# Performance work log

Hardware: AMD Instinct MI355X
Metric: run time of the kernel (lower is better)

The kernel has to match this reference:

```python
import jax, jax.numpy as jnp
import numpy as np
from jax import lax

DIM = 384
NH = 8
HD = DIM // NH
M = 16          # num_anchors
B = 16
HH = 64
WW = 64
N = HH * WW
STD = 0.02


def setup_inputs() -> dict:
    key = jax.random.key(0)
    ks = jax.random.split(key, 12)
    rn = lambda k, shape: (jax.random.normal(k, shape, jnp.float32) * STD)
    return {
        "x": jax.random.normal(ks[0], (B, N, DIM), jnp.float32),
        "H": HH,
        "W": WW,
        "saliency_w": rn(ks[1], (DIM, 1)),
        "saliency_b": jnp.zeros((1,), jnp.float32),
        "anchor_seeds": rn(ks[2], (1, M, DIM)),
        "w_q_agg": rn(ks[3], (DIM, DIM)),
        "w_kv_agg": rn(ks[4], (DIM, 2 * DIM)),
        "w_q_self": rn(ks[5], (DIM, DIM)),
        "w_kv_self": rn(ks[6], (DIM, 2 * DIM)),
        "w_q_bcast": rn(ks[7], (DIM, DIM)),
        "w_kv_bcast": rn(ks[8], (DIM, 2 * DIM)),
        "dw_kernel": rn(ks[9], (DIM, 1, 3, 3)),  # depthwise conv, OIHW with I=1
        "w_proj": rn(ks[10], (DIM, DIM)),
    }


def _mhsa(q_in, kv_in, wq, wkv):
    """Multi-head cross attention. q_in: [B,Lq,C], kv_in: [B,Lk,C]."""
    b, lq, c = q_in.shape
    lk = kv_in.shape[1]
    scale = HD ** -0.5
    q = (q_in @ wq).reshape(b, lq, NH, HD)
    kv = (kv_in @ wkv).reshape(b, lk, 2, NH, HD)
    k, v = kv[:, :, 0], kv[:, :, 1]
    attn = jnp.einsum("bqhd,bkhd->bhqk", q, k) * scale
    attn = jax.nn.softmax(attn, axis=-1)
    out = jnp.einsum("bhqk,bkhd->bqhd", attn, v).reshape(b, lq, c)
    return out


def reference(x, H, W, saliency_w, saliency_b, anchor_seeds,
              w_q_agg, w_kv_agg, w_q_self, w_kv_self,
              w_q_bcast, w_kv_bcast, dw_kernel, w_proj):
    b, n, c = x.shape
    # saliency gating
    sal = jax.nn.sigmoid(x @ saliency_w + saliency_b)  # [B,N,1]
    x_sal = x * sal
    # stage 1: anchors aggregate from saliency-gated tokens
    anchors = jnp.broadcast_to(anchor_seeds, (b, M, c))
    anchors = anchors + _mhsa(anchors, x_sal, w_q_agg, w_kv_agg)
    # stage 2: anchor self-attention
    anchors = anchors + _mhsa(anchors, anchors, w_q_self, w_kv_self)
    # stage 3: broadcast anchors back to all tokens
    global_out = _mhsa(x, anchors, w_q_bcast, w_kv_bcast)
    # depthwise 3x3 conv on the 2D token map
    x2d = x.reshape(b, H, W, c).transpose(0, 3, 1, 2)  # NCHW
    local = lax.conv_general_dilated(
        x2d, dw_kernel, window_strides=(1, 1), padding="SAME",
        feature_group_count=c,
        dimension_numbers=("NCHW", "OIHW", "NCHW"))
    local = local.transpose(0, 2, 3, 1).reshape(b, n, c)
    return (global_out + local) @ w_proj
```

## Files before the change

kernel.cpp:

```cpp
#include <hip/hip_runtime.h>
#include <hip/hip_bf16.h>

#define SCALE 0.14433756729740643f

typedef __attribute__((ext_vector_type(8))) short bf16x8;
typedef __attribute__((ext_vector_type(4))) float f32x4;

template <typename T> __device__ inline T cvt_from_f(float v);
template <> __device__ inline float cvt_from_f<float>(float v) { return v; }
template <> __device__ inline __hip_bfloat16 cvt_from_f<__hip_bfloat16>(float v) { return __float2bfloat16(v); }

__device__ inline void gload16(const void* g, void* l) {
  __builtin_amdgcn_global_load_lds((const __attribute__((address_space(1))) void*)g,
                                   (__attribute__((address_space(3))) void*)l, 16, 0, 0);
}

__device__ inline int xcd_flat(int nwg) {
  int flat = (blockIdx.z * gridDim.y + blockIdx.y) * gridDim.x + blockIdx.x;
  int per = nwg >> 3;
  return (flat & 7) * per + (flat >> 3);
}

__global__ __launch_bounds__(256) void prep(const float* __restrict__ x,
                                            const float* __restrict__ wsal,
                                            const float* __restrict__ bsal,
                                            __hip_bfloat16* __restrict__ xb,
                                            float* __restrict__ sal) {
  int wave = threadIdx.x >> 6, lane = threadIdx.x & 63;
  size_t row = (size_t)blockIdx.x * 4 + wave;
  const float* xr = x + row * 384;
  float xs[6];
  float part = 0.f;
#pragma unroll
  for (int j = 0; j < 6; j++) {
    int c = lane + 64 * j;
    xs[j] = xr[c];
    part += xs[j] * wsal[c];
  }
#pragma unroll
  for (int off = 32; off >= 1; off >>= 1) part += __shfl_xor(part, off);
  float s = 1.f / (1.f + __expf(-(part + bsal[0])));
#pragma unroll
  for (int j = 0; j < 6; j++) {
    int c = lane + 64 * j;
    xb[row * 384 + c] = __float2bfloat16(xs[j]);
  }
  if (lane == 0) sal[row] = s;
}

__global__ __launch_bounds__(256) void xtrans(const __hip_bfloat16* __restrict__ xb,
                                              __hip_bfloat16* __restrict__ xbT) {
  __shared__ short t[64][66];
  int n0 = blockIdx.x * 64, c0 = blockIdx.y * 64, b = blockIdx.z;
  int tid = threadIdx.x;
  int r = tid >> 3, c8 = tid & 7;
#pragma unroll
  for (int i = 0; i < 2; i++) {
    int row = r + i * 32;
    bf16x8 v = *(const bf16x8*)(xb + ((size_t)(b * 4096 + n0 + row)) * 384 + c0 + c8 * 8);
    unsigned int* trow = (unsigned int*)&t[row][c8 * 8];
#pragma unroll
    for (int j = 0; j < 4; j++) {
      union { unsigned int u; short s[2]; } p;
      p.s[0] = v[j * 2];
      p.s[1] = v[j * 2 + 1];
      trow[j] = p.u;
    }
  }
  __syncthreads();
#pragma unroll
  for (int i = 0; i < 2; i++) {
    int crow = r + i * 32;
    short tb[8];
#pragma unroll
    for (int j = 0; j < 8; j++) tb[j] = t[c8 * 8 + j][crow];
    *(ulonglong2*)(xbT + ((size_t)b * 384 + c0 + crow) * 4096 + n0 + c8 * 8) = *(ulonglong2*)tb;
  }
}

__global__ __launch_bounds__(256) void weights_prep(const float* __restrict__ wkv,
                                                    const float* __restrict__ wproj,
                                                    const float* __restrict__ seeds,
                                                    const float* __restrict__ wqagg,
                                                    __hip_bfloat16* __restrict__ wvlT,
                                                    __hip_bfloat16* __restrict__ bt2,
                                                    float* __restrict__ qseed) {
  __shared__ float shbuf[16 * 385];
  int bx = blockIdx.x;
  int tid = threadIdx.x;
  if (bx < 576) {
    int idx = bx * 256 + tid;
    if (idx < 384 * 384) {
      int n = idx / 384, k = idx % 384;
      wvlT[idx] = __float2bfloat16(wkv[(size_t)k * 768 + 384 + n]);
    }
  } else if (bx < 720) {
    int bx2 = bx - 576;
    int xt = bx2 % 6, yt = (bx2 / 6) % 6, zb = bx2 / 36;
    float(*t)[65] = (float(*)[65])shbuf;
    int kt = xt * 64, ct = yt * 64;
    int c = tid & 63, r4 = tid >> 6;
#pragma unroll
    for (int i = 0; i < 16; i++) {
      int r = i * 4 + r4;
      t[r][c] = wproj[(size_t)(kt + r) * 384 + ct + c];
    }
    __syncthreads();
    __hip_bfloat16 vals[16];
#pragma unroll
    for (int i = 0; i < 16; i++) vals[i] = __float2bfloat16(t[c][i * 4 + r4]);
    for (int b = zb * 4; b < zb * 4 + 4; b++) {
      __hip_bfloat16* dst = bt2 + (size_t)b * 196608;
#pragma unroll
      for (int i = 0; i < 16; i++) {
        int rr = i * 4 + r4;
        dst[(size_t)(ct + rr) * 512 + kt + c] = vals[i];
      }
    }
  } else {
    int bxq = bx - 720;
    float(*a1)[385] = (float(*)[385])shbuf;
    int cs = bxq * 16;
    for (int idx = tid; idx < 6144; idx += 256) a1[idx / 384][idx % 384] = seeds[idx];
    __syncthreads();
    int m = tid >> 4, cc = tid & 15;
    int col = cs + cc;
    const float* wp = wqagg + col;
    float acc0 = 0.f, acc1 = 0.f, acc2 = 0.f, acc3 = 0.f;
#pragma unroll 4
    for (int k = 0; k < 384; k += 4) {
      acc0 += a1[m][k] * wp[(size_t)k * 384];
      acc1 += a1[m][k + 1] * wp[(size_t)(k + 1) * 384];
      acc2 += a1[m][k + 2] * wp[(size_t)(k + 2) * 384];
      acc3 += a1[m][k + 3] * wp[(size_t)(k + 3) * 384];
    }
    qseed[m * 384 + col] = ((acc0 + acc1) + (acc2 + acc3)) * SCALE;
  }
}

template <int K, typename OT, int BSHIFT>
__global__ __launch_bounds__(256) void gemm_mfma(const __hip_bfloat16* __restrict__ A,
                                                 const __hip_bfloat16* __restrict__ BT,
                                                 OT* __restrict__ out, int Ncols,
                                                 size_t btBatchStride) {
  __shared__ __align__(16) __hip_bfloat16 Asl[128][32];
  __shared__ __align__(16) __hip_bfloat16 Bsl[128][32];
  int nf = xcd_flat(gridDim.x * gridDim.y);
  int bX = nf % gridDim.x, bY = nf / gridDim.x;
  int tid = threadIdx.x;
  int lane = tid & 63;
  int w = tid >> 6;
  int wr = w >> 1, wc = w & 1;
  int fr = lane & 15, fq = lane >> 4;
  int rowBase = bY * 128, colBase = bX * 128;
  const __hip_bfloat16* BTb = BT + (size_t)(rowBase >> BSHIFT) * btBatchStride;

  int r1 = tid >> 2, kc1 = tid & 3;
  int r2 = (tid + 256) >> 2;

  char* aB1 = (char*)Asl + (size_t)(w * 64) * 16;
  char* aB2 = (char*)Asl + (size_t)(256 + w * 64) * 16;
  char* bB1 = (char*)Bsl + (size_t)(w * 64) * 16;
  char* bB2 = (char*)Bsl + (size_t)(256 + w * 64) * 16;

  const __hip_bfloat16* a1 = A + (size_t)(rowBase + r1) * K + kc1 * 8;
  const __hip_bfloat16* a2 = A + (size_t)(rowBase + r2) * K + kc1 * 8;
  const __hip_bfloat16* b1 = BTb + (size_t)(colBase + r1) * K + kc1 * 8;
  const __hip_bfloat16* b2 = BTb + (size_t)(colBase + r2) * K + kc1 * 8;

  f32x4 acc[4][4] = {};

  for (int kk = 0; kk < K; kk += 32) {
    gload16(a1 + kk, aB1);
    gload16(a2 + kk, aB2);
    gload16(b1 + kk, bB1);
    gload16(b2 + kk, bB2);
    __syncthreads();
    bf16x8 af[4], bfv[4];
#pragma unroll
    for (int m = 0; m < 4; m++) af[m] = *(const bf16x8*)&Asl[wr * 64 + m * 16 + fr][fq * 8];
#pragma unroll
    for (int n = 0; n < 4; n++) bfv[n] = *(const bf16x8*)&Bsl[wc * 64 + n * 16 + fr][fq * 8];
#pragma unroll
    for (int m = 0; m < 4; m++)
#pragma unroll
      for (int n = 0; n < 4; n++)
        acc[m][n] = __builtin_amdgcn_mfma_f32_16x16x32_bf16(af[m], bfv[n], acc[m][n], 0, 0, 0);
    __syncthreads();
  }

#pragma unroll
  for (int m = 0; m < 4; m++) {
    int row0 = rowBase + wr * 64 + m * 16 + fq * 4;
#pragma unroll
    for (int n = 0; n < 4; n++) {
      int col = colBase + wc * 64 + n * 16 + fr;
      f32x4 v = acc[m][n];
#pragma unroll
      for (int r = 0; r < 4; r++) out[(size_t)(row0 + r) * Ncols + col] = cvt_from_f<OT>(v[r]);
    }
  }
}

__global__ __launch_bounds__(256) void gemm_out(const __hip_bfloat16* __restrict__ A,
                                                const __hip_bfloat16* __restrict__ BT,
                                                float* __restrict__ out) {
  __shared__ __align__(16) __hip_bfloat16 Asl[128][64];
  __shared__ __align__(16) __hip_bfloat16 Bsl[128][64];
  int nf = xcd_flat(1536);
  int bX = nf % 3, bY = nf / 3;
  int tid = threadIdx.x;
  int lane = tid & 63;
  int w = tid >> 6;
  int wr = w >> 1, wc = w & 1;
  int fr = lane & 15, fq = lane >> 4;
  int rowBase = bY * 128, colBase = bX * 128;
  const __hip_bfloat16* BTb = BT + (size_t)(rowBase >> 12) * (384 * 512);

  int r0 = tid >> 3, jc = tid & 7;
  int kc = jc ^ (r0 & 7);
  char* aB[4];
  char* bB[4];
  const __hip_bfloat16* a_src[4];
  const __hip_bfloat16* b_src[4];
#pragma unroll
  for (int i = 0; i < 4; i++) {
    aB[i] = (char*)Asl + (size_t)(i * 256 + w * 64) * 16;
    bB[i] = (char*)Bsl + (size_t)(i * 256 + w * 64) * 16;
    a_src[i] = A + (size_t)(rowBase + r0 + i * 32) * 512 + kc * 8;
    b_src[i] = BTb + (size_t)(colBase + r0 + i * 32) * 512 + kc * 8;
  }

  f32x4 acc[4][4] = {};

  for (int kk = 0; kk < 512; kk += 64) {
#pragma unroll
    for (int i = 0; i < 4; i++) {
      gload16(a_src[i] + kk, aB[i]);
      gload16(b_src[i] + kk, bB[i]);
    }
    __syncthreads();
#pragma unroll
    for (int half = 0; half < 2; half++) {
      bf16x8 af[4], bfv[4];
#pragma unroll
      for (int m = 0; m < 4; m++) {
        int row = wr * 64 + m * 16 + fr;
        af[m] = *(const bf16x8*)((char*)Asl + (size_t)row * 128 +
                                 (((fq + 4 * half) ^ (row & 7)) << 4));
      }
#pragma unroll
      for (int n = 0; n < 4; n++) {
        int row = wc * 64 + n * 16 + fr;
        bfv[n] = *(const bf16x8*)((char*)Bsl + (size_t)row * 128 +
                                  (((fq + 4 * half) ^ (row & 7)) << 4));
      }
#pragma unroll
      for (int m = 0; m < 4; m++)
#pragma unroll
        for (int n = 0; n < 4; n++)
          acc[m][n] = __builtin_amdgcn_mfma_f32_16x16x32_bf16(af[m], bfv[n], acc[m][n], 0, 0, 0);
    }
    __syncthreads();
  }

#pragma unroll
  for (int m = 0; m < 4; m++) {
    int row0 = rowBase + wr * 64 + m * 16 + fq * 4;
#pragma unroll
    for (int n = 0; n < 4; n++) {
      int col = colBase + wc * 64 + n * 16 + fr;
      f32x4 v = acc[m][n];
#pragma unroll
      for (int r = 0; r < 4; r++) out[(size_t)(row0 + r) * 384 + col] = v[r];
    }
  }
}

__global__ __launch_bounds__(256) void gemm_logits(const __hip_bfloat16* __restrict__ A,
                                                   const __hip_bfloat16* __restrict__ BT,
                                                   __hip_bfloat16* __restrict__ lgT,
                                                   const float* __restrict__ rowScale) {
  __shared__ __align__(16) __hip_bfloat16 Asl[128][64];
  __shared__ __align__(16) __hip_bfloat16 Bsl[128][64];
  int tid = threadIdx.x;
  int lane = tid & 63;
  int w = tid >> 6;
  int wr = w >> 1, wc = w & 1;
  int fr = lane & 15, fq = lane >> 4;
  int rowBase = blockIdx.x * 128;

  int r0 = tid >> 3, jc = tid & 7;
  int kc = jc ^ (r0 & 7);
  char* aB[4];
  char* bB[4];
  const __hip_bfloat16* a_src[4];
  const __hip_bfloat16* b_src[4];
#pragma unroll
  for (int i = 0; i < 4; i++) {
    aB[i] = (char*)Asl + (size_t)(i * 256 + w * 64) * 16;
    bB[i] = (char*)Bsl + (size_t)(i * 256 + w * 64) * 16;
    a_src[i] = A + (size_t)(rowBase + r0 + i * 32) * 384 + kc * 8;
    b_src[i] = BT + (size_t)(r0 + i * 32) * 384 + kc * 8;
  }

  f32x4 acc[4][4] = {};

  for (int kk = 0; kk < 384; kk += 64) {
#pragma unroll
    for (int i = 0; i < 4; i++) {
      gload16(a_src[i] + kk, aB[i]);
      gload16(b_src[i] + kk, bB[i]);
    }
    __syncthreads();
#pragma unroll
    for (int half = 0; half < 2; half++) {
      bf16x8 af[4], bfv[4];
#pragma unroll
      for (int m = 0; m < 4; m++) {
        int row = wr * 64 + m * 16 + fr;
        af[m] = *(const bf16x8*)((char*)Asl + (size_t)row * 128 +
                                 (((fq + 4 * half) ^ (row & 7)) << 4));
      }
#pragma unroll
      for (int n = 0; n < 4; n++) {
        int row = wc * 64 + n * 16 + fr;
        bfv[n] = *(const bf16x8*)((char*)Bsl + (size_t)row * 128 +
                                  (((fq + 4 * half) ^ (row & 7)) << 4));
      }
#pragma unroll
      for (int m = 0; m < 4; m++)
#pragma unroll
        for (int n = 0; n < 4; n++)
          acc[m][n] = __builtin_amdgcn_mfma_f32_16x16x32_bf16(af[m], bfv[n], acc[m][n], 0, 0, 0);
    }
    __syncthreads();
  }

  float sv[4][4];
#pragma unroll
  for (int m = 0; m < 4; m++)
#pragma unroll
    for (int r = 0; r < 4; r++)
      sv[m][r] = rowScale[rowBase + wr * 64 + m * 16 + fq * 4 + r];

#pragma unroll
  for (int m = 0; m < 4; m++) {
    int row0 = rowBase + wr * 64 + m * 16 + fq * 4;
    int bb = row0 >> 12;
    int n0 = row0 & 4095;
#pragma unroll
    for (int n = 0; n < 4; n++) {
      int col = wc * 64 + n * 16 + fr;
      __hip_bfloat16 tb[4];
#pragma unroll
      for (int r = 0; r < 4; r++) tb[r] = __float2bfloat16(acc[m][n][r] * sv[m][r]);
      *(unsigned long long*)(lgT + ((size_t)bb * 128 + col) * 4096 + n0) = *(unsigned long long*)tb;
    }
  }
}

__global__ __launch_bounds__(256) void softmax_rows(const __hip_bfloat16* __restrict__ lgT,
                                                    const float* __restrict__ sal,
                                                    __hip_bfloat16* __restrict__ PT) {
  int g = blockIdx.x;
  const __hip_bfloat16* row = lgT + (size_t)g * 4096;
  int tid = threadIdx.x, wv = tid >> 6, lane = tid & 63;
  __shared__ float redm[4], reds[4];
  float v[16];
  union { ulonglong2 u; __hip_bfloat16 h[8]; } L0, L1;
  L0.u = *(const ulonglong2*)(row + tid * 16);
  L1.u = *(const ulonglong2*)(row + tid * 16 + 8);
#pragma unroll
  for (int i = 0; i < 8; i++) {
    v[i] = __bfloat162float(L0.h[i]);
    v[8 + i] = __bfloat162float(L1.h[i]);
  }
  float mx = v[0];
#pragma unroll
  for (int i = 1; i < 16; i++) mx = fmaxf(mx, v[i]);
#pragma unroll
  for (int off = 1; off < 64; off <<= 1) mx = fmaxf(mx, __shfl_xor(mx, off));
  if (lane == 0) redm[wv] = mx;
  __syncthreads();
  mx = fmaxf(fmaxf(redm[0], redm[1]), fmaxf(redm[2], redm[3]));
  float s = 0.f;
#pragma unroll
  for (int i = 0; i < 16; i++) {
    v[i] = __expf(v[i] - mx);
    s += v[i];
  }
#pragma unroll
  for (int off = 1; off < 64; off <<= 1) s += __shfl_xor(s, off);
  if (lane == 0) reds[wv] = s;
  __syncthreads();
  s = (reds[0] + reds[1]) + (reds[2] + reds[3]);
  float inv = 1.f / s;
  const float* sp = sal + (size_t)(g >> 7) * 4096 + tid * 16;
  float salv[16];
#pragma unroll
  for (int i = 0; i < 4; i++) {
    float4 q = *(const float4*)(sp + i * 4);
    salv[i * 4] = q.x; salv[i * 4 + 1] = q.y; salv[i * 4 + 2] = q.z; salv[i * 4 + 3] = q.w;
  }
  __hip_bfloat16 tb[16];
#pragma unroll
  for (int i = 0; i < 16; i++) tb[i] = __float2bfloat16(v[i] * inv * salv[i]);
  __hip_bfloat16* op = PT + (size_t)g * 4096 + tid * 16;
  *(ulonglong2*)op = *(ulonglong2*)tb;
  *(ulonglong2*)(op + 8) = *(ulonglong2*)(tb + 8);
}

__global__ __launch_bounds__(256) void gemm_pvx(const __hip_bfloat16* __restrict__ PT,
                                                const __hip_bfloat16* __restrict__ xbT,
                                                float* __restrict__ pbuf) {
  __shared__ __align__(16) __hip_bfloat16 Asl[128][64];
  __shared__ __align__(16) __hip_bfloat16 Bsl[128][64];
  int nf = xcd_flat(192);
  int bX = nf % 3, bY = (nf / 3) & 15, kz = nf / 48;
  int tid = threadIdx.x;
  int lane = tid & 63;
  int w = tid >> 6;
  int wr = w >> 1, wc = w & 1;
  int fr = lane & 15, fq = lane >> 4;
  int rowBase = bY * 128, colBase = bX * 128;
  const __hip_bfloat16* BTb = xbT + (size_t)bY * 384 * 4096;

  int r0 = tid >> 3, jc = tid & 7;
  int kc = jc ^ (r0 & 7);
  char* aB[4];
  char* bB[4];
  const __hip_bfloat16* a_src[4];
  const __hip_bfloat16* b_src[4];
#pragma unroll
  for (int i = 0; i < 4; i++) {
    aB[i] = (char*)Asl + (size_t)(i * 256 + w * 64) * 16;
    bB[i] = (char*)Bsl + (size_t)(i * 256 + w * 64) * 16;
    a_src[i] = PT + (size_t)(rowBase + r0 + i * 32) * 4096 + kz * 1024 + kc * 8;
    b_src[i] = BTb + (size_t)(colBase + r0 + i * 32) * 4096 + kz * 1024 + kc * 8;
  }

  f32x4 acc[4][4] = {};

  for (int kk = 0; kk < 1024; kk += 64) {
#pragma unroll
    for (int i = 0; i < 4; i++) {
      gload16(a_src[i] + kk, aB[i]);
      gload16(b_src[i] + kk, bB[i]);
    }
    __syncthreads();
#pragma unroll
    for (int half = 0; half < 2; half++) {
      bf16x8 af[4], bfv[4];
#pragma unroll
      for (int m = 0; m < 4; m++) {
        int row = wr * 64 + m * 16 + fr;
        af[m] = *(const bf16x8*)((char*)Asl + (size_t)row * 128 +
                                 (((fq + 4 * half) ^ (row & 7)) << 4));
      }
#pragma unroll
      for (int n = 0; n < 4; n++) {
        int row = wc * 64 + n * 16 + fr;
        bfv[n] = *(const bf16x8*)((char*)Bsl + (size_t)row * 128 +
                                  (((fq + 4 * half) ^ (row & 7)) << 4));
      }
#pragma unroll
      for (int m = 0; m < 4; m++)
#pragma unroll
        for (int n = 0; n < 4; n++)
          acc[m][n] = __builtin_amdgcn_mfma_f32_16x16x32_bf16(af[m], bfv[n], acc[m][n], 0, 0, 0);
    }
    __syncthreads();
  }

  float* outz = pbuf + (size_t)kz * 786432;
#pragma unroll
  for (int m = 0; m < 4; m++) {
    int row0 = rowBase + wr * 64 + m * 16 + fq * 4;
#pragma unroll
    for (int n = 0; n < 4; n++) {
      int col = colBase + wc * 64 + n * 16 + fr;
      f32x4 v = acc[m][n];
#pragma unroll
      for (int r = 0; r < 4; r++) outz[(size_t)(row0 + r) * 384 + col] = v[r];
    }
  }
}

__global__ __launch_bounds__(256) void reduce_z(const float* __restrict__ pbuf,
                                                __hip_bfloat16* __restrict__ pvx) {
  int i4 = (blockIdx.x * 256 + threadIdx.x) * 4;
  float4 s = *(const float4*)(pbuf + i4);
#pragma unroll
  for (int z = 1; z < 4; z++) {
    float4 t = *(const float4*)(pbuf + (size_t)z * 786432 + i4);
    s.x += t.x; s.y += t.y; s.z += t.z; s.w += t.w;
  }
  __hip_bfloat16 tb[4] = {__float2bfloat16(s.x), __float2bfloat16(s.y),
                          __float2bfloat16(s.z), __float2bfloat16(s.w)};
  *(unsigned long long*)(pvx + i4) = *(unsigned long long*)tb;
}

__global__ void anch_fix(const float* __restrict__ outF, const float* __restrict__ seeds,
                         float* __restrict__ anch1) {
  int idx = blockIdx.x * 256 + threadIdx.x;
  int b = idx / 6144;
  int rem = idx - b * 6144;
  int m = rem / 384, c = rem - m * 384;
  int h = c / 48;
  anch1[idx] = seeds[rem] + outF[((size_t)b * 128 + h * 16 + m) * 384 + c];
}

__global__ void fill_wl(const float* __restrict__ wkv, const float* __restrict__ qseed,
                        __hip_bfloat16* __restrict__ wvlT) {
  int idx = blockIdx.x * 256 + threadIdx.x;
  int hm = idx / 384, ci = idx - hm * 384;
  int h = hm >> 4, m = hm & 15;
  const float* wp = wkv + (size_t)ci * 768 + h * 48;
  const float* qp = qseed + m * 384 + h * 48;
  float acc = 0.f;
#pragma unroll
  for (int d = 0; d < 48; d++) acc += wp[d] * qp[d];
  wvlT[384 * 384 + idx] = __float2bfloat16(acc);
}

__global__ __launch_bounds__(256) void kvfold(const float* __restrict__ anch2,
                                              const float* __restrict__ wkvb,
                                              const float* __restrict__ wq,
                                              const float* __restrict__ wproj,
                                              __hip_bfloat16* __restrict__ wpbT,
                                              __hip_bfloat16* __restrict__ bt2) {
  int b = blockIdx.y;
  int tid = threadIdx.x;
  __shared__ float a2s[16][385];
  __shared__ float stage[16][48];
  __shared__ __hip_bfloat16 obuf[16][264];
  bool isK = blockIdx.x < 8;
  int h = isK ? blockIdx.x : blockIdx.x - 8;
  int colBase = (isK ? 0 : 384) + h * 48;
  float scale = isK ? SCALE : 1.f;
  for (int idx = tid; idx < 6144; idx += 256) a2s[idx / 384][idx % 384] = anch2[b * 6144 + idx];
  __syncthreads();
  for (int o = tid; o < 768; o += 256) {
    int m = o / 48, d = o - m * 48;
    const float* wp = wkvb + colBase + d;
    float acc0 = 0.f, acc1 = 0.f, acc2 = 0.f, acc3 = 0.f;
#pragma unroll 4
    for (int k = 0; k < 384; k += 4) {
      acc0 += a2s[m][k] * wp[(size_t)k * 768];
      acc1 += a2s[m][k + 1] * wp[(size_t)(k + 1) * 768];
      acc2 += a2s[m][k + 2] * wp[(size_t)(k + 2) * 768];
      acc3 += a2s[m][k + 3] * wp[(size_t)(k + 3) * 768];
    }
    stage[m][d] = ((acc0 + acc1) + (acc2 + acc3)) * scale;
  }
  __syncthreads();
  if (isK) {
    for (int kbase = 0; kbase < 384; kbase += 256) {
      int chunk = (kbase == 0) ? 256 : 128;
      if (tid < chunk) {
        int k = kbase + tid;
        const float4* wp = (const float4*)(wq + (size_t)k * 384 + h * 48);
        float acc[16] = {};
#pragma unroll
        for (int dq = 0; dq < 12; dq++) {
          float4 wv = wp[dq];
#pragma unroll
          for (int m = 0; m < 16; m++)
            acc[m] += stage[m][dq * 4] * wv.x + stage[m][dq * 4 + 1] * wv.y +
                      stage[m][dq * 4 + 2] * wv.z + stage[m][dq * 4 + 3] * wv.w;
        }
#pragma unroll
        for (int m = 0; m < 16; m++) obuf[m][tid] = __float2bfloat16(acc[m]);
      }
      __syncthreads();
      for (int widx = tid; widx < 16 * chunk; widx += 256) {
        int m = widx / chunk, kk = widx - m * chunk;
        wpbT[(size_t)b * 49152 + (size_t)(h * 16 + m) * 384 + kbase + kk] = obuf[m][kk];
      }
      __syncthreads();
    }
  } else {
    for (int cp = tid; cp < 384; cp += 256) {
      float acc[16] = {};
      for (int d = 0; d < 48; d++) {
        float wv = wproj[(size_t)(h * 48 + d) * 384 + cp];
#pragma unroll
        for (int m = 0; m < 16; m++) acc[m] += stage[m][d] * wv;
      }
      __hip_bfloat16 tb[16];
#pragma unroll
      for (int m = 0; m < 16; m++) tb[m] = __float2bfloat16(acc[m]);
      __hip_bfloat16* dst = bt2 + (size_t)b * 196608 + (size_t)cp * 512 + 384 + h * 16;
      *(ulonglong2*)dst = *(ulonglong2*)tb;
      *(ulonglong2*)(dst + 8) = *(ulonglong2*)(tb + 8);
    }
  }
}

__global__ __launch_bounds__(256) void pgemm(const __hip_bfloat16* __restrict__ A,
                                             const __hip_bfloat16* __restrict__ wpbT,
                                             __hip_bfloat16* __restrict__ A2) {
  __shared__ __align__(16) __hip_bfloat16 Asl[128][64];
  __shared__ __align__(16) __hip_bfloat16 Bsl[128][64];
  int tid = threadIdx.x;
  int lane = tid & 63;
  int w = tid >> 6;
  int wr = w >> 1, wc = w & 1;
  int fr = lane & 15, fq = lane >> 4;
  int rowBase = blockIdx.x * 128;
  const __hip_bfloat16* BTb = wpbT + (size_t)(rowBase >> 12) * (128 * 384);

  int r0 = tid >> 3, jc = tid & 7;
  int kc = jc ^ (r0 & 7);
  char* aB[4];
  char* bB[4];
  const __hip_bfloat16* a_src[4];
  const __hip_bfloat16* b_src[4];
#pragma unroll
  for (int i = 0; i < 4; i++) {
    aB[i] = (char*)Asl + (size_t)(i * 256 + w * 64) * 16;
    bB[i] = (char*)Bsl + (size_t)(i * 256 + w * 64) * 16;
    a_src[i] = A + (size_t)(rowBase + r0 + i * 32) * 384 + kc * 8;
    b_src[i] = BTb + (size_t)(r0 + i * 32) * 384 + kc * 8;
  }

  f32x4 acc[4][4] = {};

  for (int kk = 0; kk < 384; kk += 64) {
#pragma unroll
    for (int i = 0; i < 4; i++) {
      gload16(a_src[i] + kk, aB[i]);
      gload16(b_src[i] + kk, bB[i]);
    }
    __syncthreads();
#pragma unroll
    for (int half = 0; half < 2; half++) {
      bf16x8 af[4], bfv[4];
#pragma unroll
      for (int m = 0; m < 4; m++) {
        int row = wr * 64 + m * 16 + fr;
        af[m] = *(const bf16x8*)((char*)Asl + (size_t)row * 128 +
                                 (((fq + 4 * half) ^ (row & 7)) << 4));
      }
#pragma unroll
      for (int n = 0; n < 4; n++) {
        int row = wc * 64 + n * 16 + fr;
        bfv[n] = *(const bf16x8*)((char*)Bsl + (size_t)row * 128 +
                                  (((fq + 4 * half) ^ (row & 7)) << 4));
      }
#pragma unroll
      for (int m = 0; m < 4; m++)
#pragma unroll
        for (int n = 0; n < 4; n++)
          acc[m][n] = __builtin_amdgcn_mfma_f32_16x16x32_bf16(af[m], bfv[n], acc[m][n], 0, 0, 0);
    }
    __syncthreads();
  }

#pragma unroll
  for (int m = 0; m < 4; m++) {
    int row0 = rowBase + wr * 64 + m * 16 + fq * 4;
#pragma unroll
    for (int n = 0; n < 4; n++) {
      int col = wc * 64 + n * 16 + fr;
      f32x4 v = acc[m][n];
      f32x4 mx = v;
#pragma unroll
      for (int off = 1; off < 16; off <<= 1)
#pragma unroll
        for (int r = 0; r < 4; r++) mx[r] = fmaxf(mx[r], __shfl_xor(mx[r], off));
      f32x4 e;
#pragma unroll
      for (int r = 0; r < 4; r++) e[r] = __expf(v[r] - mx[r]);
      f32x4 s = e;
#pragma unroll
      for (int off = 1; off < 16; off <<= 1)
#pragma unroll
        for (int r = 0; r < 4; r++) s[r] += __shfl_xor(s[r], off);
#pragma unroll
      for (int r = 0; r < 4; r++)
        A2[(size_t)(row0 + r) * 512 + 384 + col] = __float2bfloat16(e[r] / s[r]);
    }
  }
}

__global__ __launch_bounds__(256) void dwconv3(const __hip_bfloat16* __restrict__ xb,
                                               const float* __restrict__ dwk,
                                               __hip_bfloat16* __restrict__ A2) {
  int b = blockIdx.y;
  int y = blockIdx.x;
  int w = threadIdx.x >> 6, lane = threadIdx.x & 63;
  int c0 = lane * 6;
  int x0 = w * 16;
  float kw[9][6];
#pragma unroll
  for (int ki = 0; ki < 9; ki++)
#pragma unroll
    for (int i = 0; i < 6; i++) kw[ki][i] = dwk[(c0 + i) * 9 + ki];

  const __hip_bfloat16* base = xb + ((size_t)(b * 4096 + y * 64)) * 384 + c0;
  bool yv[3];
#pragma unroll
  for (int t = 0; t < 3; t++) {
    int yy = y + t - 1;
    yv[t] = (yy >= 0 && yy < 64);
  }

  float colL[3][6], colC[3][6], colR[3][6];
  auto loadcol = [&](float (&dst)[3][6], int x) {
#pragma unroll
    for (int t = 0; t < 3; t++) {
      if (yv[t]) {
        const __hip_bfloat16* p = base + ((size_t)(t - 1) * 64 + x) * 384;
#pragma unroll
        for (int i = 0; i < 6; i++) dst[t][i] = __bfloat162float(p[i]);
      } else {
#pragma unroll
        for (int i = 0; i < 6; i++) dst[t][i] = 0.f;
      }
    }
  };

  if (x0 == 0) {
#pragma unroll
    for (int t = 0; t < 3; t++)
#pragma unroll
      for (int i = 0; i < 6; i++) colL[t][i] = 0.f;
  } else {
    loadcol(colL, x0 - 1);
  }
  loadcol(colC, x0);

  for (int step = 0; step < 16; step++) {
    int x = x0 + step;
    if (x + 1 < 64) {
      loadcol(colR, x + 1);
    } else {
#pragma unroll
      for (int t = 0; t < 3; t++)
#pragma unroll
        for (int i = 0; i < 6; i++) colR[t][i] = 0.f;
    }
    float acc[6];
#pragma unroll
    for (int i = 0; i < 6; i++) {
      float a = 0.f;
#pragma unroll
      for (int t = 0; t < 3; t++)
        a += colL[t][i] * kw[t * 3 + 0][i] + colC[t][i] * kw[t * 3 + 1][i] +
             colR[t][i] * kw[t * 3 + 2][i];
      acc[i] = a;
    }
    __hip_bfloat16 tb[6];
#pragma unroll
    for (int i = 0; i < 6; i++) tb[i] = __float2bfloat16(acc[i]);
    __hip_bfloat16* gp = A2 + ((size_t)(b * 4096 + y * 64 + x)) * 512 + c0;
    *(unsigned int*)(gp) = *(unsigned int*)(tb);
    *(unsigned int*)(gp + 2) = *(unsigned int*)(tb + 2);
    *(unsigned int*)(gp + 4) = *(unsigned int*)(tb + 4);
#pragma unroll
    for (int t = 0; t < 3; t++)
#pragma unroll
      for (int i = 0; i < 6; i++) {
        colL[t][i] = colC[t][i];
        colC[t][i] = colR[t][i];
      }
  }
}

__global__ __launch_bounds__(256) void anchor_proj_qkv(const float* __restrict__ A,
                                                       const float* __restrict__ Wq,
                                                       const float* __restrict__ Wkv,
                                                       float* __restrict__ q_out,
                                                       float* __restrict__ kv_out) {
  bool isQ = blockIdx.x < 24;
  int bx = isQ ? blockIdx.x : blockIdx.x - 24;
  const float* W = isQ ? Wq : Wkv;
  float* outp = isQ ? q_out : kv_out;
  int wstride = isQ ? 384 : 768;
  float scale = isQ ? SCALE : 1.f;
  int cs = bx * 16;
  int b = blockIdx.y;
  __shared__ float a1[16][385];
  int tid = threadIdx.x;
  for (int idx = tid; idx < 6144; idx += 256) a1[idx / 384][idx % 384] = A[b * 6144 + idx];
  __syncthreads();
  int m = tid >> 4, cc = tid & 15;
  int col = cs + cc;
  const float* wp = W + col;
  float acc0 = 0.f, acc1 = 0.f, acc2 = 0.f, acc3 = 0.f;
#pragma unroll 4
  for (int k = 0; k < 384; k += 4) {
    acc0 += a1[m][k] * wp[(size_t)k * wstride];
    acc1 += a1[m][k + 1] * wp[(size_t)(k + 1) * wstride];
    acc2 += a1[m][k + 2] * wp[(size_t)(k + 2) * wstride];
    acc3 += a1[m][k + 3] * wp[(size_t)(k + 3) * wstride];
  }
  float acc = ((acc0 + acc1) + (acc2 + acc3)) * scale;
  outp[((size_t)b * 16 + m) * wstride + col] = acc;
}

__global__ void self_attn(const float* __restrict__ qsf, const float* __restrict__ kvs,
                          const float* __restrict__ anch1, float* __restrict__ anch2) {
  int h = blockIdx.x & 7, b = blockIdx.x >> 3;
  __shared__ float qs[16][48], ks[16][48], vs[16][48], p[16][17];
  int tid = threadIdx.x;
  for (int idx = tid; idx < 768; idx += 256) {
    int m = idx / 48, d = idx % 48;
    qs[m][d] = qsf[(b * 16 + m) * 384 + h * 48 + d];
    ks[m][d] = kvs[(b * 16 + m) * 768 + h * 48 + d];
    vs[m][d] = kvs[(b * 16 + m) * 768 + 384 + h * 48 + d];
  }
  __syncthreads();
  {
    int mq = tid >> 4, mk = tid & 15;
    float acc = 0.f;
    for (int d = 0; d < 48; d++) acc += qs[mq][d] * ks[mk][d];
    p[mq][mk] = acc;
  }
  __syncthreads();
  if (tid < 16) {
    float mx = -1e30f;
    for (int mk = 0; mk < 16; mk++) mx = fmaxf(mx, p[tid][mk]);
    float sum = 0.f;
    for (int mk = 0; mk < 16; mk++) {
      float e = __expf(p[tid][mk] - mx);
      p[tid][mk] = e;
      sum += e;
    }
    float inv = 1.f / sum;
    for (int mk = 0; mk < 16; mk++) p[tid][mk] *= inv;
  }
  __syncthreads();
  for (int idx = tid; idx < 768; idx += 256) {
    int m = idx / 48, d = idx % 48;
    float acc = 0.f;
    for (int mk = 0; mk < 16; mk++) acc += p[m][mk] * vs[mk][d];
    int c = h * 48 + d;
    anch2[(b * 16 + m) * 384 + c] = anch1[(b * 16 + m) * 384 + c] + acc;
  }
}

extern "C" void kernel_launch(void* const* d_in, const int* in_sizes, int n_in,
                              void* d_out, int out_size, void* d_ws, size_t ws_size,
                              hipStream_t stream) {
  (void)in_sizes; (void)n_in; (void)out_size; (void)ws_size;
  const float* x = (const float*)d_in[0];
  const float* wsal = (const float*)d_in[3];
  const float* bsal = (const float*)d_in[4];
  const float* seeds = (const float*)d_in[5];
  const float* w_q_agg = (const float*)d_in[6];
  const float* w_kv_agg = (const float*)d_in[7];
  const float* w_q_self = (const float*)d_in[8];
  const float* w_kv_self = (const float*)d_in[9];
  const float* w_q_bcast = (const float*)d_in[10];
  const float* w_kv_bcast = (const float*)d_in[11];
  const float* dwk = (const float*)d_in[12];
  const float* w_proj = (const float*)d_in[13];
  float* out = (float*)d_out;

  char* ws = (char*)d_ws;
  size_t off = 0;
  auto take = [&](size_t bytes) -> void* {
    void* p = ws + off;
    off += (bytes + 255) & ~(size_t)255;
    return p;
  };
  __hip_bfloat16* xb = (__hip_bfloat16*)take(50331648);
  __hip_bfloat16* xbT = (__hip_bfloat16*)take(50331648);
  char* R = (char*)take(67108864);
  __hip_bfloat16* PT = (__hip_bfloat16*)take(16777216);
  __hip_bfloat16* pvx = (__hip_bfloat16*)take(1572864);
  float* outF = (float*)take(3145728);
  float* qseed = (float*)take(24576);
  float* sal = (float*)take(262144);
  float* anch1 = (float*)take(393216);
  float* anch2 = (float*)take(393216);
  float* q_self = (float*)take(393216);
  float* kv_self = (float*)take(786432);
  __hip_bfloat16* wvlT = (__hip_bfloat16*)take(393216);
  __hip_bfloat16* wpbT = (__hip_bfloat16*)take(1572864);
  __hip_bfloat16* bt2 = (__hip_bfloat16*)take(6291456);
  __hip_bfloat16* logitsT = (__hip_bfloat16*)R;
  float* pbuf = (float*)R;
  __hip_bfloat16* A2 = (__hip_bfloat16*)R;

  prep<<<16384, 256, 0, stream>>>(x, wsal, bsal, xb, sal);
  xtrans<<<dim3(64, 6, 16), 256, 0, stream>>>(xb, xbT);
  weights_prep<<<744, 256, 0, stream>>>(w_kv_agg, w_proj, seeds, w_q_agg, wvlT, bt2, qseed);
  fill_wl<<<192, 256, 0, stream>>>(w_kv_agg, qseed, wvlT);
  gemm_logits<<<512, 256, 0, stream>>>(xb, wvlT + 384 * 384, logitsT, sal);
  softmax_rows<<<2048, 256, 0, stream>>>(logitsT, sal, PT);
  gemm_pvx<<<dim3(3, 16, 4), 256, 0, stream>>>(PT, xbT, pbuf);
  reduce_z<<<768, 256, 0, stream>>>(pbuf, pvx);
  gemm_mfma<384, float, 12><<<dim3(3, 16), 256, 0, stream>>>(pvx, wvlT, outF, 384, 0);
  anch_fix<<<384, 256, 0, stream>>>(outF, seeds, anch1);
  anchor_proj_qkv<<<dim3(72, 16), 256, 0, stream>>>(anch1, w_q_self, w_kv_self, q_self, kv_self);
  self_attn<<<128, 256, 0, stream>>>(q_self, kv_self, anch1, anch2);
  kvfold<<<dim3(16, 16), 256, 0, stream>>>(anch2, w_kv_bcast, w_q_bcast, w_proj, wpbT, bt2);
  pgemm<<<512, 256, 0, stream>>>(xb, wpbT, A2);
  dwconv3<<<dim3(64, 16), 256, 0, stream>>>(xb, dwk, A2);
  gemm_out<<<dim3(3, 512), 256, 0, stream>>>(A2, bt2, out);
}
```

Baseline: 320.2 us.

## Merge independent kernels into shared launches to cut launch count

```diff
diff --git a/kernel.cpp b/kernel.cpp
--- a/kernel.cpp
+++ b/kernel.cpp
@@ -48,44 +48,14 @@
   if (lane == 0) sal[row] = s;
 }
 
-__global__ __launch_bounds__(256) void xtrans(const __hip_bfloat16* __restrict__ xb,
-                                              __hip_bfloat16* __restrict__ xbT) {
-  __shared__ short t[64][66];
-  int n0 = blockIdx.x * 64, c0 = blockIdx.y * 64, b = blockIdx.z;
-  int tid = threadIdx.x;
-  int r = tid >> 3, c8 = tid & 7;
-#pragma unroll
-  for (int i = 0; i < 2; i++) {
-    int row = r + i * 32;
-    bf16x8 v = *(const bf16x8*)(xb + ((size_t)(b * 4096 + n0 + row)) * 384 + c0 + c8 * 8);
-    unsigned int* trow = (unsigned int*)&t[row][c8 * 8];
-#pragma unroll
-    for (int j = 0; j < 4; j++) {
-      union { unsigned int u; short s[2]; } p;
-      p.s[0] = v[j * 2];
-      p.s[1] = v[j * 2 + 1];
-      trow[j] = p.u;
-    }
-  }
-  __syncthreads();
-#pragma unroll
-  for (int i = 0; i < 2; i++) {
-    int crow = r + i * 32;
-    short tb[8];
-#pragma unroll
-    for (int j = 0; j < 8; j++) tb[j] = t[c8 * 8 + j][crow];
-    *(ulonglong2*)(xbT + ((size_t)b * 384 + c0 + crow) * 4096 + n0 + c8 * 8) = *(ulonglong2*)tb;
-  }
-}
-
 __global__ __launch_bounds__(256) void weights_prep(const float* __restrict__ wkv,
                                                     const float* __restrict__ wproj,
                                                     const float* __restrict__ seeds,
                                                     const float* __restrict__ wqagg,
                                                     __hip_bfloat16* __restrict__ wvlT,
-                                                    __hip_bfloat16* __restrict__ bt2,
-                                                    float* __restrict__ qseed) {
+                                                    __hip_bfloat16* __restrict__ bt2) {
   __shared__ float shbuf[16 * 385];
+  __shared__ float qsl[16][48];
   int bx = blockIdx.x;
   int tid = threadIdx.x;
   if (bx < 576) {
@@ -118,23 +88,29 @@
       }
     }
   } else {
-    int bxq = bx - 720;
+    int h = bx - 720;
     float(*a1)[385] = (float(*)[385])shbuf;
-    int cs = bxq * 16;
     for (int idx = tid; idx < 6144; idx += 256) a1[idx / 384][idx % 384] = seeds[idx];
     __syncthreads();
-    int m = tid >> 4, cc = tid & 15;
-    int col = cs + cc;
-    const float* wp = wqagg + col;
-    float acc0 = 0.f, acc1 = 0.f, acc2 = 0.f, acc3 = 0.f;
-#pragma unroll 4
-    for (int k = 0; k < 384; k += 4) {
-      acc0 += a1[m][k] * wp[(size_t)k * 384];
-      acc1 += a1[m][k + 1] * wp[(size_t)(k + 1) * 384];
-      acc2 += a1[m][k + 2] * wp[(size_t)(k + 2) * 384];
-      acc3 += a1[m][k + 3] * wp[(size_t)(k + 3) * 384];
-    }
-    qseed[m * 384 + col] = ((acc0 + acc1) + (acc2 + acc3)) * SCALE;
+    for (int o = tid; o < 768; o += 256) {
+      int m = o / 48, d = o - m * 48;
+      const float* wp = wqagg + h * 48 + d;
+      float acc0 = 0.f, acc1 = 0.f;
+      for (int k = 0; k < 384; k += 2) {
+        acc0 += a1[m][k] * wp[(size_t)k * 384];
+        acc1 += a1[m][k + 1] * wp[(size_t)(k + 1) * 384];
+      }
+      qsl[m][d] = (acc0 + acc1) * SCALE;
+    }
+    __syncthreads();
+    for (int idx = tid; idx < 6144; idx += 256) {
+      int m = idx / 384, ci = idx - m * 384;
+      const float* wp = wkv + (size_t)ci * 768 + h * 48;
+      float acc = 0.f;
+#pragma unroll
+      for (int d = 0; d < 48; d++) acc += wp[d] * qsl[m][d];
+      wvlT[384 * 384 + (size_t)(h * 16 + m) * 384 + ci] = __float2bfloat16(acc);
+    }
   }
 }
 
@@ -277,13 +253,45 @@
   }
 }
 
-__global__ __launch_bounds__(256) void gemm_logits(const __hip_bfloat16* __restrict__ A,
-                                                   const __hip_bfloat16* __restrict__ BT,
-                                                   __hip_bfloat16* __restrict__ lgT,
-                                                   const float* __restrict__ rowScale) {
+__global__ __launch_bounds__(256) void glx(const __hip_bfloat16* __restrict__ A,
+                                           const __hip_bfloat16* __restrict__ BT,
+                                           __hip_bfloat16* __restrict__ lgT,
+                                           const float* __restrict__ rowScale,
+                                           __hip_bfloat16* __restrict__ xbT) {
   __shared__ __align__(16) __hip_bfloat16 Asl[128][64];
   __shared__ __align__(16) __hip_bfloat16 Bsl[128][64];
   int tid = threadIdx.x;
+  if (blockIdx.x >= 512) {
+    int b2 = blockIdx.x - 512;
+    int n0 = (b2 & 63) * 64;
+    int c0 = ((b2 >> 6) % 6) * 64;
+    int b = b2 / 384;
+    short(*t)[66] = (short(*)[66])Asl;
+    int r = tid >> 3, c8 = tid & 7;
+#pragma unroll
+    for (int i = 0; i < 2; i++) {
+      int row = r + i * 32;
+      bf16x8 v = *(const bf16x8*)(A + ((size_t)(b * 4096 + n0 + row)) * 384 + c0 + c8 * 8);
+      unsigned int* trow = (unsigned int*)&t[row][c8 * 8];
+#pragma unroll
+      for (int j = 0; j < 4; j++) {
+        union { unsigned int u; short s[2]; } p;
+        p.s[0] = v[j * 2];
+        p.s[1] = v[j * 2 + 1];
+        trow[j] = p.u;
+      }
+    }
+    __syncthreads();
+#pragma unroll
+    for (int i = 0; i < 2; i++) {
+      int crow = r + i * 32;
+      short tb[8];
+#pragma unroll
+      for (int j = 0; j < 8; j++) tb[j] = t[c8 * 8 + j][crow];
+      *(ulonglong2*)(xbT + ((size_t)b * 384 + c0 + crow) * 4096 + n0 + c8 * 8) = *(ulonglong2*)tb;
+    }
+    return;
+  }
   int lane = tid & 63;
   int w = tid >> 6;
   int wr = w >> 1, wc = w & 1;
@@ -509,19 +517,6 @@
   int m = rem / 384, c = rem - m * 384;
   int h = c / 48;
   anch1[idx] = seeds[rem] + outF[((size_t)b * 128 + h * 16 + m) * 384 + c];
-}
-
-__global__ void fill_wl(const float* __restrict__ wkv, const float* __restrict__ qseed,
-                        __hip_bfloat16* __restrict__ wvlT) {
-  int idx = blockIdx.x * 256 + threadIdx.x;
-  int hm = idx / 384, ci = idx - hm * 384;
-  int h = hm >> 4, m = hm & 15;
-  const float* wp = wkv + (size_t)ci * 768 + h * 48;
-  const float* qp = qseed + m * 384 + h * 48;
-  float acc = 0.f;
-#pragma unroll
-  for (int d = 0; d < 48; d++) acc += wp[d] * qp[d];
-  wvlT[384 * 384 + idx] = __float2bfloat16(acc);
 }
 
 __global__ __launch_bounds__(256) void kvfold(const float* __restrict__ anch2,
@@ -598,12 +593,95 @@
   }
 }
 
-__global__ __launch_bounds__(256) void pgemm(const __hip_bfloat16* __restrict__ A,
-                                             const __hip_bfloat16* __restrict__ wpbT,
-                                             __hip_bfloat16* __restrict__ A2) {
+__global__ __launch_bounds__(256) void pgemm_dw(const __hip_bfloat16* __restrict__ A,
+                                                const __hip_bfloat16* __restrict__ wpbT,
+                                                const float* __restrict__ dwk,
+                                                __hip_bfloat16* __restrict__ A2) {
   __shared__ __align__(16) __hip_bfloat16 Asl[128][64];
   __shared__ __align__(16) __hip_bfloat16 Bsl[128][64];
   int tid = threadIdx.x;
+  if (blockIdx.x >= 512) {
+    int b2 = blockIdx.x - 512;
+    int y = b2 & 63, b = b2 >> 6;
+    int w = tid >> 6, lane = tid & 63;
+    int c0 = lane * 6;
+    int x0 = w * 16;
+    float kw[9][6];
+#pragma unroll
+    for (int ki = 0; ki < 9; ki++)
+#pragma unroll
+      for (int i = 0; i < 6; i++) kw[ki][i] = dwk[(c0 + i) * 9 + ki];
+
+    const __hip_bfloat16* base = A + ((size_t)(b * 4096 + y * 64)) * 384 + c0;
+    bool yv[3];
+#pragma unroll
+    for (int t = 0; t < 3; t++) {
+      int yy = y + t - 1;
+      yv[t] = (yy >= 0 && yy < 64);
+    }
+
+    float colL[3][6], colC[3][6], colR[3][6];
+    auto loadcol = [&](float (&dst)[3][6], int x) {
+#pragma unroll
+      for (int t = 0; t < 3; t++) {
+        if (yv[t]) {
+          const __hip_bfloat16* p = base + ((size_t)(t - 1) * 64 + x) * 384;
+#pragma unroll
+          for (int i = 0; i < 6; i++) dst[t][i] = __bfloat162float(p[i]);
+        } else {
+#pragma unroll
+          for (int i = 0; i < 6; i++) dst[t][i] = 0.f;
+        }
+      }
+    };
+
+    if (x0 == 0) {
+#pragma unroll
+      for (int t = 0; t < 3; t++)
+#pragma unroll
+        for (int i = 0; i < 6; i++) colL[t][i] = 0.f;
+    } else {
+      loadcol(colL, x0 - 1);
+    }
+    loadcol(colC, x0);
+
+    for (int step = 0; step < 16; step++) {
+      int x = x0 + step;
+      if (x + 1 < 64) {
+        loadcol(colR, x + 1);
+      } else {
+#pragma unroll
+        for (int t = 0; t < 3; t++)
+#pragma unroll
+          for (int i = 0; i < 6; i++) colR[t][i] = 0.f;
+      }
+      float acc[6];
+#pragma unroll
+      for (int i = 0; i < 6; i++) {
+        float a = 0.f;
+#pragma unroll
+        for (int t = 0; t < 3; t++)
+          a += colL[t][i] * kw[t * 3 + 0][i] + colC[t][i] * kw[t * 3 + 1][i] +
+               colR[t][i] * kw[t * 3 + 2][i];
+        acc[i] = a;
+      }
+      __hip_bfloat16 tb[6];
+#pragma unroll
+      for (int i = 0; i < 6; i++) tb[i] = __float2bfloat16(acc[i]);
+      __hip_bfloat16* gp = A2 + ((size_t)(b * 4096 + y * 64 + x)) * 512 + c0;
+      *(unsigned int*)(gp) = *(unsigned int*)(tb);
+      *(unsigned int*)(gp + 2) = *(unsigned int*)(tb + 2);
+      *(unsigned int*)(gp + 4) = *(unsigned int*)(tb + 4);
+#pragma unroll
+      for (int t = 0; t < 3; t++)
+#pragma unroll
+        for (int i = 0; i < 6; i++) {
+          colL[t][i] = colC[t][i];
+          colC[t][i] = colR[t][i];
+        }
+    }
+    return;
+  }
   int lane = tid & 63;
   int w = tid >> 6;
   int wr = w >> 1, wc = w & 1;
@@ -682,90 +760,6 @@
       for (int r = 0; r < 4; r++)
         A2[(size_t)(row0 + r) * 512 + 384 + col] = __float2bfloat16(e[r] / s[r]);
     }
-  }
-}
-
-__global__ __launch_bounds__(256) void dwconv3(const __hip_bfloat16* __restrict__ xb,
-                                               const float* __restrict__ dwk,
-                                               __hip_bfloat16* __restrict__ A2) {
-  int b = blockIdx.y;
-  int y = blockIdx.x;
-  int w = threadIdx.x >> 6, lane = threadIdx.x & 63;
-  int c0 = lane * 6;
-  int x0 = w * 16;
-  float kw[9][6];
-#pragma unroll
-  for (int ki = 0; ki < 9; ki++)
-#pragma unroll
-    for (int i = 0; i < 6; i++) kw[ki][i] = dwk[(c0 + i) * 9 + ki];
-
-  const __hip_bfloat16* base = xb + ((size_t)(b * 4096 + y * 64)) * 384 + c0;
-  bool yv[3];
-#pragma unroll
-  for (int t = 0; t < 3; t++) {
-    int yy = y + t - 1;
-    yv[t] = (yy >= 0 && yy < 64);
-  }
-
-  float colL[3][6], colC[3][6], colR[3][6];
-  auto loadcol = [&](float (&dst)[3][6], int x) {
-#pragma unroll
-    for (int t = 0; t < 3; t++) {
-      if (yv[t]) {
-        const __hip_bfloat16* p = base + ((size_t)(t - 1) * 64 + x) * 384;
-#pragma unroll
-        for (int i = 0; i < 6; i++) dst[t][i] = __bfloat162float(p[i]);
-      } else {
-#pragma unroll
-        for (int i = 0; i < 6; i++) dst[t][i] = 0.f;
-      }
-    }
-  };
-
-  if (x0 == 0) {
-#pragma unroll
-    for (int t = 0; t < 3; t++)
-#pragma unroll
-      for (int i = 0; i < 6; i++) colL[t][i] = 0.f;
-  } else {
-    loadcol(colL, x0 - 1);
-  }
-  loadcol(colC, x0);
-
-  for (int step = 0; step < 16; step++) {
-    int x = x0 + step;
-    if (x + 1 < 64) {
-      loadcol(colR, x + 1);
-    } else {
-#pragma unroll
-      for (int t = 0; t < 3; t++)
-#pragma unroll
-        for (int i = 0; i < 6; i++) colR[t][i] = 0.f;
-    }
-    float acc[6];
-#pragma unroll
-    for (int i = 0; i < 6; i++) {
-      float a = 0.f;
-#pragma unroll
-      for (int t = 0; t < 3; t++)
-        a += colL[t][i] * kw[t * 3 + 0][i] + colC[t][i] * kw[t * 3 + 1][i] +
-             colR[t][i] * kw[t * 3 + 2][i];
-      acc[i] = a;
-    }
-    __hip_bfloat16 tb[6];
-#pragma unroll
-    for (int i = 0; i < 6; i++) tb[i] = __float2bfloat16(acc[i]);
-    __hip_bfloat16* gp = A2 + ((size_t)(b * 4096 + y * 64 + x)) * 512 + c0;
-    *(unsigned int*)(gp) = *(unsigned int*)(tb);
-    *(unsigned int*)(gp + 2) = *(unsigned int*)(tb + 2);
-    *(unsigned int*)(gp + 4) = *(unsigned int*)(tb + 4);
-#pragma unroll
-    for (int t = 0; t < 3; t++)
-#pragma unroll
-      for (int i = 0; i < 6; i++) {
-        colL[t][i] = colC[t][i];
-        colC[t][i] = colR[t][i];
-      }
   }
 }
 
@@ -873,7 +867,6 @@
   __hip_bfloat16* PT = (__hip_bfloat16*)take(16777216);
   __hip_bfloat16* pvx = (__hip_bfloat16*)take(1572864);
   float* outF = (float*)take(3145728);
-  float* qseed = (float*)take(24576);
   float* sal = (float*)take(262144);
   float* anch1 = (float*)take(393216);
   float* anch2 = (float*)take(393216);
@@ -887,10 +880,8 @@
   __hip_bfloat16* A2 = (__hip_bfloat16*)R;
 
   prep<<<16384, 256, 0, stream>>>(x, wsal, bsal, xb, sal);
-  xtrans<<<dim3(64, 6, 16), 256, 0, stream>>>(xb, xbT);
-  weights_prep<<<744, 256, 0, stream>>>(w_kv_agg, w_proj, seeds, w_q_agg, wvlT, bt2, qseed);
-  fill_wl<<<192, 256, 0, stream>>>(w_kv_agg, qseed, wvlT);
-  gemm_logits<<<512, 256, 0, stream>>>(xb, wvlT + 384 * 384, logitsT, sal);
+  weights_prep<<<728, 256, 0, stream>>>(w_kv_agg, w_proj, seeds, w_q_agg, wvlT, bt2);
+  glx<<<6656, 256, 0, stream>>>(xb, wvlT + 384 * 384, logitsT, sal, xbT);
   softmax_rows<<<2048, 256, 0, stream>>>(logitsT, sal, PT);
   gemm_pvx<<<dim3(3, 16, 4), 256, 0, stream>>>(PT, xbT, pbuf);
   reduce_z<<<768, 256, 0, stream>>>(pbuf, pvx);
@@ -899,7 +890,6 @@
   anchor_proj_qkv<<<dim3(72, 16), 256, 0, stream>>>(anch1, w_q_self, w_kv_self, q_self, kv_self);
   self_attn<<<128, 256, 0, stream>>>(q_self, kv_self, anch1, anch2);
   kvfold<<<dim3(16, 16), 256, 0, stream>>>(anch2, w_kv_bcast, w_q_bcast, w_proj, wpbT, bt2);
-  pgemm<<<512, 256, 0, stream>>>(xb, wpbT, A2);
-  dwconv3<<<dim3(64, 16), 256, 0, stream>>>(xb, dwk, A2);
+  pgemm_dw<<<1536, 256, 0, stream>>>(xb, wpbT, dwk, A2);
   gemm_out<<<dim3(3, 512), 256, 0, stream>>>(A2, bt2, out);
 }
```

New measurement: 345.1 us. 1.08x slower.
